# Performance work log

Hardware: AMD Instinct MI355X
Metric: run time of the kernel (lower is better)

## Reference

```python
import jax, jax.numpy as jnp
import numpy as np

D = 512
H = 8
W = 128  # window_size
HD = D // H
EPS = 1e-5


def _layernorm(x, g, b):
    mu = jnp.mean(x, axis=-1, keepdims=True)
    var = jnp.mean(jnp.square(x - mu), axis=-1, keepdims=True)
    return (x - mu) * jax.lax.rsqrt(var + EPS) * g + b


def setup_inputs() -> dict:
    key = jax.random.key(0)
    ks = jax.random.split(key, 6)
    B, S = 4, 8192
    src = jax.random.normal(ks[0], (B, S, D), jnp.float32)
    sc = 1.0 / np.sqrt(D)
    in_proj_w = jax.random.normal(ks[1], (3 * D, D), jnp.float32) * sc
    in_proj_b = jnp.zeros((3 * D,), jnp.float32)
    out_w = jax.random.normal(ks[2], (D, D), jnp.float32) * sc
    out_b = jnp.zeros((D,), jnp.float32)
    w1 = jax.random.normal(ks[3], (4 * D, D), jnp.float32) * sc
    b1 = jnp.zeros((4 * D,), jnp.float32)
    w2 = jax.random.normal(ks[4], (D, 4 * D), jnp.float32) * (1.0 / np.sqrt(4 * D))
    b2 = jnp.zeros((D,), jnp.float32)
    return {
        'src': src,
        'in_proj_w': in_proj_w, 'in_proj_b': in_proj_b,
        'out_w': out_w, 'out_b': out_b,
        'ln1_g': jnp.ones((D,), jnp.float32), 'ln1_b': jnp.zeros((D,), jnp.float32),
        'w1': w1, 'b1': b1, 'w2': w2, 'b2': b2,
        'ln2_g': jnp.ones((D,), jnp.float32), 'ln2_b': jnp.zeros((D,), jnp.float32),
    }


def reference(src, in_proj_w, in_proj_b, out_w, out_b, ln1_g, ln1_b,
              w1, b1, w2, b2, ln2_g, ln2_b):
    B, S, _ = src.shape
    nW = S // W
    x = src.reshape(B, nW, W, D)  # block-diagonal windows
    # packed qkv projection (torch MultiheadAttention in_proj)
    qkv = jnp.einsum('bnwd,ed->bnwe', x, in_proj_w) + in_proj_b
    q, k, v = jnp.split(qkv, 3, axis=-1)
    q = q.reshape(B, nW, W, H, HD)
    k = k.reshape(B, nW, W, H, HD)
    v = v.reshape(B, nW, W, H, HD)
    scores = jnp.einsum('bnqhd,bnkhd->bnhqk', q, k) / np.sqrt(HD)
    probs = jax.nn.softmax(scores, axis=-1)
    attn = jnp.einsum('bnhqk,bnkhd->bnqhd', probs, v).reshape(B, nW, W, D)
    attn = jnp.einsum('bnwd,ed->bnwe', attn, out_w) + out_b
    x = _layernorm(x + attn, ln1_g, ln1_b)
    ff = jnp.einsum('bnwf,df->bnwd', jax.nn.relu(jnp.einsum('bnwd,fd->bnwf', x, w1) + b1), w2) + b2
    x = _layernorm(x + ff, ln2_g, ln2_b)
    return x.reshape(B, S, D)
```

## Files before the change

### kernel.cpp

```cpp
#include <hip/hip_runtime.h>
#include <hip/hip_bf16.h>
#include <math.h>

typedef __bf16 bf16;
typedef bf16 bf16x8 __attribute__((ext_vector_type(8)));
typedef bf16 bf16x4 __attribute__((ext_vector_type(4)));
typedef float f32x4 __attribute__((ext_vector_type(4)));

#define MFMA16(a, b, c) __builtin_amdgcn_mfma_f32_16x16x32_bf16(a, b, c, 0, 0, 0)

__device__ __forceinline__ uint32_t swz(uint32_t base, uint32_t row, uint32_t rs, uint32_t cb) {
    return base + row * rs + (((cb >> 4) ^ (row & 7u)) << 4) + (cb & 15u);
}

__device__ __forceinline__ void gload16(const void* g, void* l) {
    __builtin_amdgcn_global_load_lds((const __attribute__((address_space(1))) void*)g,
                                     (__attribute__((address_space(3))) void*)l, 16, 0, 0);
}


__global__ void wcvt_kernel(const float* __restrict__ w0, const float* __restrict__ w1o,
                            const float* __restrict__ w1f, const float* __restrict__ w2f,
                            bf16* __restrict__ o) {
    int i = blockIdx.x * blockDim.x + threadIdx.x;
    const float* s;
    int soff, doff;
    if (i < 98304)        { int e = i * 8; s = w0; soff = e; doff = e; }
    else if (i < 131072)  { int e = (i - 98304) * 8; s = w1o; soff = e; doff = 786432 + e; }
    else if (i < 262144)  {
        int u = i - 131072;
        int tile = u >> 11, c = (u >> 9) & 3, nn = u & 511;
        int n = (tile >> 4) * 512 + nn;
        int k = (tile & 15) * 32 + c * 8;
        s = w1f; soff = n * 512 + k; doff = 1048576 + u * 8;
    } else {
        int u = i - 262144;
        int t = u >> 11, c = (u >> 9) & 3, nn = u & 511;
        int k = t * 32 + c * 8;
        s = w2f; soff = nn * 2048 + k; doff = 2097152 + u * 8;
    }
    float4 v0 = *(const float4*)(s + soff);
    float4 v1 = *(const float4*)(s + soff + 4);
    bf16x8 h = { (bf16)v0.x, (bf16)v0.y, (bf16)v0.z, (bf16)v0.w,
                 (bf16)v1.x, (bf16)v1.y, (bf16)v1.z, (bf16)v1.w };
    *(bf16x8*)(o + doff) = h;
}

__global__ void xcvt_kernel(float* __restrict__ src) {
    int row = blockIdx.x * 4 + (threadIdx.x >> 6);
    int l = threadIdx.x & 63;
    float* rp = src + (size_t)row * 512 + l * 8;
    float4 v0 = *(const float4*)rp;
    float4 v1 = *(const float4*)(rp + 4);
    asm volatile("s_waitcnt vmcnt(0)" ::: "memory");
    bf16x8 h = { (bf16)v0.x, (bf16)v0.y, (bf16)v0.z, (bf16)v0.w,
                 (bf16)v1.x, (bf16)v1.y, (bf16)v1.z, (bf16)v1.w };
    *(bf16x8*)((bf16*)(src + (size_t)row * 512) + l * 8) = h;
}

extern "C" __global__ __launch_bounds__(256, 3)
void qkv_kernel(const char* __restrict__ xb, const bf16* __restrict__ Wqkv,
                const float* __restrict__ bqkv, char* __restrict__ qOb,
                char* __restrict__ kvb) {
    extern __shared__ char smem[];
    const int tid = threadIdx.x;
    const int wid = tid >> 6, lane = tid & 63, l16 = lane & 15, quad = lane >> 4;
    const int wm = wid >> 1, wn = wid & 1;
    const int rb = blockIdx.x, cb = blockIdx.y;
    f32x4 acc[4][4];
#pragma unroll
    for (int i = 0; i < 4; ++i)
#pragma unroll
        for (int nt = 0; nt < 4; ++nt) acc[i][nt] = (f32x4){0.f, 0.f, 0.f, 0.f};

#pragma unroll 1
    for (int kstep = 0; kstep < 8; ++kstep) {
        {
            int lr = tid >> 1, half = tid & 1;
            const char* g = (const char*)(Wqkv + (size_t)(cb * 128 + lr) * 512 + kstep * 64 + half * 32);
#pragma unroll
            for (int c = 0; c < 4; ++c) {
                bf16x8 v = *(const bf16x8*)(g + c * 16);
                *(bf16x8*)(smem + swz(0, lr, 128, half * 64 + c * 16)) = v;
            }
        }
        __syncthreads();
#pragma unroll
        for (int k16 = 0; k16 < 2; ++k16) {
            bf16x8 a[4];
#pragma unroll
            for (int i = 0; i < 4; ++i) {
                int row = rb * 128 + wm * 64 + i * 16 + l16;
                a[i] = *(const bf16x8*)(xb + (size_t)row * 2048 + (kstep * 64 + k16 * 32 + quad * 8) * 2);
            }
#pragma unroll
            for (int nt = 0; nt < 4; ++nt) {
                bf16x8 b = *(bf16x8*)(smem + swz(0, wn * 64 + nt * 16 + l16, 128, k16 * 64 + quad * 16));
#pragma unroll
                for (int i = 0; i < 4; ++i) acc[i][nt] = MFMA16(a[i], b, acc[i][nt]);
            }
        }
        __syncthreads();
    }
    const uint32_t wb = (uint32_t)wid * 8192;
#pragma unroll
    for (int nt = 0; nt < 4; ++nt) {
        float bias = bqkv[cb * 128 + wn * 64 + nt * 16 + l16];
#pragma unroll
        for (int i = 0; i < 4; ++i)
#pragma unroll
            for (int r = 0; r < 4; ++r)
                *(bf16*)(smem + swz(wb, i * 16 + quad * 4 + r, 128, (nt * 16 + l16) * 2)) =
                    (bf16)(acc[i][nt][r] + bias);
    }
    asm volatile("s_waitcnt lgkmcnt(0)" ::: "memory");
    const int region = cb >> 2;
#pragma unroll
    for (int c = 0; c < 8; ++c) {
        int lr = c * 8 + (lane >> 3), ch = lane & 7;
        bf16x8 v = *(bf16x8*)(smem + swz(wb, lr, 128, ch * 16));
        int row_g = rb * 128 + wm * 64 + lr;
        int colb = (cb * 128 + wn * 64) * 2 + ch * 16;
        if (region == 0)      *(bf16x8*)(qOb + (size_t)row_g * 1024 + colb) = v;
        else if (region == 1) *(bf16x8*)(kvb + (size_t)row_g * 2048 + (colb - 1024)) = v;
        else                  *(bf16x8*)(kvb + (size_t)row_g * 2048 + 1024 + (colb - 2048)) = v;
    }
}

#define AVT 0u
#define ASCR 16384u
extern "C" __global__ __launch_bounds__(512, 4)
void attn_kernel(char* __restrict__ qOb, const char* __restrict__ kvb) {
    extern __shared__ char smem[];
    const int tid = threadIdx.x;
    const int wid = tid >> 6, lane = tid & 63, l16 = lane & 15, quad = lane >> 4;
    const int win = blockIdx.x >> 3, head = blockIdx.x & 7;
    const size_t wrow0 = (size_t)win * 128;
    f32x4 zero4 = { 0.f, 0.f, 0.f, 0.f };

    {
        int key = tid >> 2, d0 = (tid & 3) * 16;
        const char* vs = kvb + (wrow0 + key) * 2048 + 1024 + head * 128 + d0 * 2;
#pragma unroll
        for (int j = 0; j < 2; ++j) {
            bf16x8 v = *(const bf16x8*)(vs + j * 16);
#pragma unroll
            for (int e = 0; e < 8; ++e)
                *(bf16*)(smem + swz(AVT, d0 + j * 8 + e, 256, key * 2)) = v[e];
        }
    }
    __syncthreads();

    bf16x8 qf[2];
#pragma unroll
    for (int ks = 0; ks < 2; ++ks)
        qf[ks] = *(const bf16x8*)(qOb + (wrow0 + wid * 16 + l16) * 1024 + head * 128 + ks * 64 + quad * 16);

    f32x4 sa[8];
#pragma unroll
    for (int nt = 0; nt < 8; ++nt) sa[nt] = zero4;
#pragma unroll
    for (int nt = 0; nt < 8; ++nt)
#pragma unroll
        for (int ks = 0; ks < 2; ++ks) {
            bf16x8 kb = *(const bf16x8*)(kvb + (wrow0 + nt * 16 + l16) * 2048 + head * 128 + ks * 64 + quad * 16);
            sa[nt] = MFMA16(qf[ks], kb, sa[nt]);
        }
#pragma unroll
    for (int nt = 0; nt < 8; ++nt) sa[nt] *= 0.125f;
#pragma unroll
    for (int r = 0; r < 4; ++r) {
        float m = sa[0][r];
#pragma unroll
        for (int nt = 1; nt < 8; ++nt) m = fmaxf(m, sa[nt][r]);
#pragma unroll
        for (int sft = 1; sft < 16; sft <<= 1) m = fmaxf(m, __shfl_xor(m, sft, 64));
        float s = 0.f;
#pragma unroll
        for (int nt = 0; nt < 8; ++nt) {
            float e = __expf(sa[nt][r] - m);
            sa[nt][r] = e;
            s += e;
        }
#pragma unroll
        for (int sft = 1; sft < 16; sft <<= 1) s += __shfl_xor(s, sft, 64);
        float inv = 1.0f / s;
#pragma unroll
        for (int nt = 0; nt < 8; ++nt) sa[nt][r] *= inv;
    }

    const uint32_t sb = ASCR + (uint32_t)wid * 2048;
    bf16x8 pf[4];
#pragma unroll
    for (int hf = 0; hf < 2; ++hf) {
#pragma unroll
        for (int nt = 0; nt < 4; ++nt)
#pragma unroll
            for (int r = 0; r < 4; ++r)
                *(bf16*)(smem + swz(sb, quad * 4 + r, 128, (nt * 16 + l16) * 2)) = (bf16)sa[hf * 4 + nt][r];
        asm volatile("s_waitcnt lgkmcnt(0)" ::: "memory");
#pragma unroll
        for (int ks = 0; ks < 2; ++ks)
            pf[hf * 2 + ks] = *(bf16x8*)(smem + swz(sb, l16, 128, ks * 64 + quad * 16));
        asm volatile("s_waitcnt lgkmcnt(0)" ::: "memory");
    }

    f32x4 ov[4];
#pragma unroll
    for (int nt = 0; nt < 4; ++nt) {
        ov[nt] = zero4;
#pragma unroll
        for (int ks = 0; ks < 4; ++ks) {
            bf16x8 vb = *(bf16x8*)(smem + swz(AVT, nt * 16 + l16, 256, ks * 64 + quad * 16));
            ov[nt] = MFMA16(pf[ks], vb, ov[nt]);
        }
    }
#pragma unroll
    for (int hf = 0; hf < 2; ++hf) {
#pragma unroll
        for (int nt = 0; nt < 2; ++nt)
#pragma unroll
            for (int r = 0; r < 4; ++r)
                *(bf16*)(smem + swz(sb, quad * 4 + r, 128, (nt * 16 + l16) * 2)) = (bf16)ov[hf * 2 + nt][r];
        asm volatile("s_waitcnt lgkmcnt(0)" ::: "memory");
        {
            int row = lane >> 2, ch = lane & 3;
            bf16x8 v = *(bf16x8*)(smem + swz(sb, row, 128, ch * 16));
            *(bf16x8*)(qOb + (wrow0 + wid * 16 + row) * 1024 + head * 128 + hf * 64 + ch * 16) = v;
        }
        asm volatile("s_waitcnt lgkmcnt(0)" ::: "memory");
    }
}

extern "C" __global__ __launch_bounds__(256, 2)
void outproj_kernel(char* __restrict__ srcb, const char* __restrict__ qOb,
                    const bf16* __restrict__ Wout, const float* __restrict__ bout,
                    const float* __restrict__ g1, const float* __restrict__ be1) {
    extern __shared__ char smem[];
    const int tid = threadIdx.x;
    const int wid = tid >> 6, lane = tid & 63, l16 = lane & 15, quad = lane >> 4;
    const int mb = blockIdx.x;
    f32x4 acc[32];
#pragma unroll
    for (int nt = 0; nt < 32; ++nt) acc[nt] = (f32x4){0.f, 0.f, 0.f, 0.f};

#pragma unroll 1
    for (int kstep = 0; kstep < 8; ++kstep) {
        {
            int n0 = tid * 2;
#pragma unroll
            for (int rr = 0; rr < 2; ++rr) {
                int n = n0 + rr;
                const char* g = (const char*)(Wout + (size_t)n * 512 + kstep * 64);
#pragma unroll
                for (int c = 0; c < 8; ++c) {
                    bf16x8 v = *(const bf16x8*)(g + c * 16);
                    *(bf16x8*)(smem + swz(0, n, 128, c * 16)) = v;
                }
            }
        }
        __syncthreads();
#pragma unroll
        for (int k16 = 0; k16 < 2; ++k16) {
            bf16x8 a = *(const bf16x8*)(qOb + (size_t)(mb * 64 + wid * 16 + l16) * 1024 +
                                        (kstep * 64 + k16 * 32 + quad * 8) * 2);
#pragma unroll
            for (int nt = 0; nt < 32; ++nt) {
                bf16x8 b = *(bf16x8*)(smem + swz(0, nt * 16 + l16, 128, k16 * 64 + quad * 16));
                acc[nt] = MFMA16(a, b, acc[nt]);
            }
        }
        __syncthreads();
    }
#pragma unroll
    for (int nt = 0; nt < 32; ++nt) {
        int col = nt * 16 + l16;
        float bb = bout[col];
#pragma unroll
        for (int r = 0; r < 4; ++r) {
            int row = mb * 64 + wid * 16 + quad * 4 + r;
            float xv = (float)*(const bf16*)(srcb + (size_t)row * 2048 + col * 2);
            acc[nt][r] += bb + xv;
        }
    }
    const uint32_t wb = (uint32_t)wid * 16384;
#pragma unroll
    for (int r = 0; r < 4; ++r) {
        float s = 0.f, s2 = 0.f;
#pragma unroll
        for (int nt = 0; nt < 32; ++nt) {
            float v = acc[nt][r];
            s += v;
            s2 += v * v;
        }
#pragma unroll
        for (int sft = 1; sft < 16; sft <<= 1) {
            s += __shfl_xor(s, sft, 64);
            s2 += __shfl_xor(s2, sft, 64);
        }
        float mu = s * (1.0f / 512.0f);
        float var = s2 * (1.0f / 512.0f) - mu * mu;
        float rstd = rsqrtf(var + 1e-5f);
#pragma unroll
        for (int nt = 0; nt < 32; ++nt) {
            int col = nt * 16 + l16;
            float v = (acc[nt][r] - mu) * rstd * g1[col] + be1[col];
            *(bf16*)(smem + swz(wb, quad * 4 + r, 1024, col * 2)) = (bf16)v;
        }
    }
    asm volatile("s_waitcnt lgkmcnt(0)" ::: "memory");
#pragma unroll
    for (int t = 0; t < 16; ++t) {
        int row = (t >> 2) * 4 + (lane >> 4);
        int ch = (t & 3) * 16 + l16;
        bf16x8 v = *(bf16x8*)(smem + swz(wb, row, 1024, ch * 16));
        *(bf16x8*)(srcb + (size_t)(mb * 64 + wid * 16 + row) * 2048 + 1024 + ch * 16) = v;
    }
}

extern "C" __global__ __launch_bounds__(512, 2)
void ff1_kernel(char* __restrict__ srcb, const char* __restrict__ W1p,
                const float* __restrict__ b1, char* __restrict__ doutb,
                char* __restrict__ wsOb) {
    extern __shared__ char smem[];
    const int tid = threadIdx.x;
    const int w = tid >> 6, lane = tid & 63, l16 = lane & 15, quad = lane >> 4;
    const int wm = w >> 2, wn = w & 3;
    const int mb = blockIdx.x, cb = blockIdx.y;

    f32x4 acc[4][8];
#pragma unroll
    for (int i = 0; i < 4; ++i)
#pragma unroll
        for (int nt = 0; nt < 8; ++nt) acc[i][nt] = (f32x4){0.f, 0.f, 0.f, 0.f};

#define FF1_STAGE(buf, t)                                                              \
    {                                                                                  \
        int ca = w >> 1, rg = w & 1;             \
        gload16(srcb + (size_t)(mb * 128 + rg * 64 + lane) * 2048 + 1024 + (t) * 64 + ca * 16, \
                smem + (uint32_t)(buf) * 8192u + ca * 2048 + rg * 1024);               \
        _Pragma("unroll")                                                              \
        for (int j = 0; j < 4; ++j) {      \
            int idx = w * 4 + j, c = idx >> 3, ng = idx & 7;                           \
            gload16(W1p + (size_t)(cb * 16 + (t)) * 32768 + c * 8192 + ng * 1024 + lane * 16, \
                    smem + 16384u + (uint32_t)(buf) * 32768u + (uint32_t)c * 8192 + (uint32_t)ng * 1024); \
        }                                                                              \
    }

    FF1_STAGE(0, 0);
    __syncthreads();

#pragma unroll 1
    for (int t = 0; t < 16; ++t) {
        if (t < 15) FF1_STAGE((t + 1) & 1, t + 1);
        const uint32_t A0 = (uint32_t)(t & 1) * 8192u;
        const uint32_t B0 = 16384u + (uint32_t)(t & 1) * 32768u;
        bf16x8 a[4];
#pragma unroll
        for (int i = 0; i < 4; ++i)
            a[i] = *(const bf16x8*)(smem + A0 + quad * 2048 + (wm * 64 + i * 16 + l16) * 16);
#pragma unroll
        for (int nt = 0; nt < 8; ++nt) {
            bf16x8 b = *(const bf16x8*)(smem + B0 + quad * 8192 + (wn * 128 + nt * 16 + l16) * 16);
#pragma unroll
            for (int i = 0; i < 4; ++i) acc[i][nt] = MFMA16(a[i], b, acc[i][nt]);
        }
        __syncthreads();
    }
#undef FF1_STAGE

    const uint32_t sb = 16384u + (uint32_t)w * 4096u;
#pragma unroll
    for (int i = 0; i < 4; ++i) {
#pragma unroll
        for (int nt = 0; nt < 8; ++nt) {
            float bb = b1[cb * 512 + wn * 128 + nt * 16 + l16];
#pragma unroll
            for (int r = 0; r < 4; ++r)
                *(bf16*)(smem + swz(sb, quad * 4 + r, 256, (nt * 16 + l16) * 2)) =
                    (bf16)fmaxf(acc[i][nt][r] + bb, 0.0f);
        }
        asm volatile("s_waitcnt lgkmcnt(0)" ::: "memory");
#pragma unroll
        for (int j = 0; j < 4; ++j) {
            int uu = j * 64 + lane;
            int row = uu >> 4, ch = uu & 15;
            bf16x8 v = *(bf16x8*)(smem + swz(sb, row, 256, ch * 16));
            size_t row_g = (size_t)(mb * 128 + wm * 64 + i * 16 + row);
            int nb2 = wn * 256 + ch * 16;
            if (cb < 2)       *(bf16x8*)(doutb + row_g * 2048 + cb * 1024 + nb2) = v;
            else if (cb == 2) *(bf16x8*)(srcb + row_g * 2048 + nb2) = v;
            else              *(bf16x8*)(wsOb + row_g * 1024 + nb2) = v;
        }
        asm volatile("s_waitcnt lgkmcnt(0)" ::: "memory");
    }
}

extern "C" __global__ __launch_bounds__(512, 2)
void ff2_kernel(char* __restrict__ doutb, const char* __restrict__ srcb,
                const char* __restrict__ wsOb, const char* __restrict__ W2p,
                const float* __restrict__ b2, const float* __restrict__ g2,
                const float* __restrict__ be2) {
    extern __shared__ char smem[];
    const int tid = threadIdx.x;
    const int w = tid >> 6, lane = tid & 63, l16 = lane & 15, quad = lane >> 4;
    const int wm = w >> 2, wn = w & 3;
    const int mb = blockIdx.x;

    f32x4 acc[4][8];
#pragma unroll
    for (int i = 0; i < 4; ++i)
#pragma unroll
        for (int nt = 0; nt < 8; ++nt) acc[i][nt] = (f32x4){0.f, 0.f, 0.f, 0.f};

#define FF2_STAGE(buf, t)                                                              \
    {                                                                                  \
        const char* hb; int rstride, koffb;                                            \
        if ((t) < 32)      { hb = doutb; rstride = 2048; koffb = (t) * 64; }           \
        else if ((t) < 48) { hb = srcb;  rstride = 2048; koffb = ((t) - 32) * 64; }    \
        else               { hb = wsOb;  rstride = 1024; koffb = ((t) - 48) * 64; }    \
        int ca = w >> 1, rg = w & 1;           \
        gload16(hb + (size_t)(mb * 128 + rg * 64 + lane) * rstride + koffb + ca * 16,  \
                smem + (uint32_t)(buf) * 8192u + ca * 2048 + rg * 1024);               \
        _Pragma("unroll")                                                              \
        for (int j = 0; j < 4; ++j) {      \
            int idx = w * 4 + j, c = idx >> 3, ng = idx & 7;                           \
            gload16(W2p + (size_t)(t) * 32768 + c * 8192 + ng * 1024 + lane * 16,      \
                    smem + 16384u + (uint32_t)(buf) * 32768u + (uint32_t)c * 8192 + (uint32_t)ng * 1024); \
        }                                                                              \
    }

    FF2_STAGE(0, 0);
    __syncthreads();

#pragma unroll 1
    for (int t = 0; t < 64; ++t) {
        if (t < 63) FF2_STAGE((t + 1) & 1, t + 1);
        const uint32_t A0 = (uint32_t)(t & 1) * 8192u;
        const uint32_t B0 = 16384u + (uint32_t)(t & 1) * 32768u;
        bf16x8 a[4];
#pragma unroll
        for (int i = 0; i < 4; ++i)
            a[i] = *(const bf16x8*)(smem + A0 + quad * 2048 + (wm * 64 + i * 16 + l16) * 16);
#pragma unroll
        for (int nt = 0; nt < 8; ++nt) {
            bf16x8 b = *(const bf16x8*)(smem + B0 + quad * 8192 + (wn * 128 + nt * 16 + l16) * 16);
#pragma unroll
            for (int i = 0; i < 4; ++i) acc[i][nt] = MFMA16(a[i], b, acc[i][nt]);
        }
        __syncthreads();
    }
#undef FF2_STAGE

#pragma unroll
    for (int nt = 0; nt < 8; ++nt) {
        int col = wn * 128 + nt * 16 + l16;
        float bb = b2[col];
#pragma unroll
        for (int i = 0; i < 4; ++i)
#pragma unroll
            for (int r = 0; r < 4; ++r) {
                int row = mb * 128 + wm * 64 + i * 16 + quad * 4 + r;
                float x1v = (float)*(const bf16*)(srcb + (size_t)row * 2048 + 1024 + col * 2);
                acc[i][nt][r] += bb + x1v;
            }
    }
    float ps[4][4], ps2[4][4];
#pragma unroll
    for (int i = 0; i < 4; ++i)
#pragma unroll
        for (int r = 0; r < 4; ++r) {
            float s = 0.f, s2 = 0.f;
#pragma unroll
            for (int nt = 0; nt < 8; ++nt) {
                float v = acc[i][nt][r];
                s += v;
                s2 += v * v;
            }
#pragma unroll
            for (int sft = 1; sft < 16; sft <<= 1) {
                s += __shfl_xor(s, sft, 64);
                s2 += __shfl_xor(s2, sft, 64);
            }
            ps[i][r] = s;
            ps2[i][r] = s2;
        }
    if (l16 == 0) {
#pragma unroll
        for (int i = 0; i < 4; ++i)
#pragma unroll
            for (int r = 0; r < 4; ++r) {
                int row_l = wm * 64 + i * 16 + quad * 4 + r;
                *(float*)(smem + row_l * 32 + wn * 8) = ps[i][r];
                *(float*)(smem + row_l * 32 + wn * 8 + 4) = ps2[i][r];
            }
    }
    __syncthreads();
#pragma unroll
    for (int i = 0; i < 4; ++i)
#pragma unroll
        for (int r = 0; r < 4; ++r) {
            int row_l = wm * 64 + i * 16 + quad * 4 + r;
            float S = 0.f, S2 = 0.f;
#pragma unroll
            for (int w4 = 0; w4 < 4; ++w4) {
                S += *(const float*)(smem + row_l * 32 + w4 * 8);
                S2 += *(const float*)(smem + row_l * 32 + w4 * 8 + 4);
            }
            float mu = S * (1.0f / 512.0f);
            float var = S2 * (1.0f / 512.0f) - mu * mu;
            float rstd = rsqrtf(var + 1e-5f);
            size_t row = (size_t)(mb * 128 + row_l);
#pragma unroll
            for (int nt = 0; nt < 8; ++nt) {
                int col = wn * 128 + nt * 16 + l16;
                *(float*)(doutb + row * 2048 + col * 4) =
                    (acc[i][nt][r] - mu) * rstd * g2[col] + be2[col];
            }
        }
}

extern "C" void kernel_launch(void* const* d_in, const int* in_sizes, int n_in,
                              void* d_out, int out_size, void* d_ws, size_t ws_size,
                              hipStream_t stream) {
    (void)in_sizes; (void)n_in; (void)out_size; (void)ws_size;
    float* src = (float*)d_in[0];
    const float* ipw = (const float*)d_in[1];
    const float* ipb = (const float*)d_in[2];
    const float* ow  = (const float*)d_in[3];
    const float* ob  = (const float*)d_in[4];
    const float* g1  = (const float*)d_in[5];
    const float* be1 = (const float*)d_in[6];
    const float* w1  = (const float*)d_in[7];
    const float* b1  = (const float*)d_in[8];
    const float* w2  = (const float*)d_in[9];
    const float* b2  = (const float*)d_in[10];
    const float* g2  = (const float*)d_in[11];
    const float* be2 = (const float*)d_in[12];
    bf16* ws = (bf16*)d_ws;
    char* srcb = (char*)src;
    char* doutb = (char*)d_out;
    char* qOb = (char*)d_ws + 6291456;

    wcvt_kernel<<<1536, 256, 0, stream>>>(ipw, ow, w1, w2, ws);
    xcvt_kernel<<<8192, 256, 0, stream>>>(src);

    hipFuncSetAttribute((const void*)qkv_kernel, hipFuncAttributeMaxDynamicSharedMemorySize, 32768);
    hipFuncSetAttribute((const void*)attn_kernel, hipFuncAttributeMaxDynamicSharedMemorySize, 32768);
    hipFuncSetAttribute((const void*)outproj_kernel, hipFuncAttributeMaxDynamicSharedMemorySize, 65536);
    hipFuncSetAttribute((const void*)ff1_kernel, hipFuncAttributeMaxDynamicSharedMemorySize, 81920);
    hipFuncSetAttribute((const void*)ff2_kernel, hipFuncAttributeMaxDynamicSharedMemorySize, 81920);

    qkv_kernel<<<dim3(256, 12), 256, 32768, stream>>>(srcb, ws, ipb, qOb, doutb);
    attn_kernel<<<2048, 512, 32768, stream>>>(qOb, doutb);
    outproj_kernel<<<512, 256, 65536, stream>>>(srcb, qOb, ws + 786432, ob, g1, be1);
    ff1_kernel<<<dim3(256, 4), 512, 81920, stream>>>(srcb, (const char*)(ws + 1048576), b1, doutb, qOb);
    ff2_kernel<<<256, 512, 81920, stream>>>(doutb, srcb, qOb, (const char*)(ws + 2097152), b2, g2, be2);
}
```

Baseline: 595.9 us.

## Rewrite QKV and out-proj GEMMs with pre-tiled weights and double-buffered async LDS loads

The QKV and output-projection weights are now pre-packed into a K-tile-major bf16 layout during conversion. Both GEMMs switch to 512-thread blocks with 128x512 output tiles, staging A and B through double-buffered LDS using direct global-to-LDS loads. The next K tile is prefetched while MFMAs run on the current one. Out-proj also gains a cross-wave LDS reduction for the LayerNorm row statistics. In exchange, each block uses more LDS (80KB) and more accumulators, and the QKV grid drops from 3072 to 768 blocks, which may lower occupancy and leave some CUs underused.

```diff
diff --git a/kernel.cpp b/kernel.cpp
--- a/kernel.cpp
+++ b/kernel.cpp
@@ -19,15 +19,24 @@
 }
 
 
-__global__ void wcvt_kernel(const float* __restrict__ w0, const float* __restrict__ w1o,
+__global__ void wcvt_kernel(const float* __restrict__ wqkv, const float* __restrict__ wout,
                             const float* __restrict__ w1f, const float* __restrict__ w2f,
                             bf16* __restrict__ o) {
     int i = blockIdx.x * blockDim.x + threadIdx.x;
     const float* s;
     int soff, doff;
-    if (i < 98304)        { int e = i * 8; s = w0; soff = e; doff = e; }
-    else if (i < 131072)  { int e = (i - 98304) * 8; s = w1o; soff = e; doff = 786432 + e; }
-    else if (i < 262144)  {
+    if (i < 98304) {
+        int u = i;
+        int tile = u >> 11, c = (u >> 9) & 3, nn = u & 511;
+        int n = (tile >> 4) * 512 + nn;
+        int k = (tile & 15) * 32 + c * 8;
+        s = wqkv; soff = n * 512 + k; doff = u * 8;
+    } else if (i < 131072) {
+        int u = i - 98304;
+        int tile = u >> 11, c = (u >> 9) & 3, nn = u & 511;
+        int k = tile * 32 + c * 8;
+        s = wout; soff = nn * 512 + k; doff = 786432 + u * 8;
+    } else if (i < 262144) {
         int u = i - 131072;
         int tile = u >> 11, c = (u >> 9) & 3, nn = u & 511;
         int n = (tile >> 4) * 512 + nn;
@@ -58,72 +67,81 @@
     *(bf16x8*)((bf16*)(src + (size_t)row * 512) + l * 8) = h;
 }
 
-extern "C" __global__ __launch_bounds__(256, 3)
-void qkv_kernel(const char* __restrict__ xb, const bf16* __restrict__ Wqkv,
+extern "C" __global__ __launch_bounds__(512, 2)
+void qkv_kernel(const char* __restrict__ xb, const char* __restrict__ Wqkvp,
                 const float* __restrict__ bqkv, char* __restrict__ qOb,
                 char* __restrict__ kvb) {
     extern __shared__ char smem[];
     const int tid = threadIdx.x;
-    const int wid = tid >> 6, lane = tid & 63, l16 = lane & 15, quad = lane >> 4;
-    const int wm = wid >> 1, wn = wid & 1;
-    const int rb = blockIdx.x, cb = blockIdx.y;
-    f32x4 acc[4][4];
+    const int w = tid >> 6, lane = tid & 63, l16 = lane & 15, quad = lane >> 4;
+    const int wm = w >> 2, wn = w & 3;
+    const int mb = blockIdx.x, cb = blockIdx.y;
+
+    f32x4 acc[4][8];
 #pragma unroll
     for (int i = 0; i < 4; ++i)
 #pragma unroll
-        for (int nt = 0; nt < 4; ++nt) acc[i][nt] = (f32x4){0.f, 0.f, 0.f, 0.f};
+        for (int nt = 0; nt < 8; ++nt) acc[i][nt] = (f32x4){0.f, 0.f, 0.f, 0.f};
+
+#define QKV_STAGE(buf, t)                                                              \
+    {                                                                                  \
+        int ca = w >> 1, rg = w & 1;           \
+        gload16(xb + (size_t)(mb * 128 + rg * 64 + lane) * 2048 + (t) * 64 + ca * 16,  \
+                smem + (uint32_t)(buf) * 8192u + ca * 2048 + rg * 1024);               \
+        _Pragma("unroll")                                                              \
+        for (int j = 0; j < 4; ++j) {      \
+            int idx = w * 4 + j, c = idx >> 3, ng = idx & 7;                           \
+            gload16(Wqkvp + (size_t)(cb * 16 + (t)) * 32768 + c * 8192 + ng * 1024 + lane * 16, \
+                    smem + 16384u + (uint32_t)(buf) * 32768u + (uint32_t)c * 8192 + (uint32_t)ng * 1024); \
+        }                                                                              \
+    }
+
+    QKV_STAGE(0, 0);
+    __syncthreads();
 
 #pragma unroll 1
-    for (int kstep = 0; kstep < 8; ++kstep) {
-        {
-            int lr = tid >> 1, half = tid & 1;
-            const char* g = (const char*)(Wqkv + (size_t)(cb * 128 + lr) * 512 + kstep * 64 + half * 32);
-#pragma unroll
-            for (int c = 0; c < 4; ++c) {
-                bf16x8 v = *(const bf16x8*)(g + c * 16);
-                *(bf16x8*)(smem + swz(0, lr, 128, half * 64 + c * 16)) = v;
-            }
+    for (int t = 0; t < 16; ++t) {
+        if (t < 15) QKV_STAGE((t + 1) & 1, t + 1);
+        const uint32_t A0 = (uint32_t)(t & 1) * 8192u;
+        const uint32_t B0 = 16384u + (uint32_t)(t & 1) * 32768u;
+        bf16x8 a[4];
+#pragma unroll
+        for (int i = 0; i < 4; ++i)
+            a[i] = *(const bf16x8*)(smem + A0 + quad * 2048 + (wm * 64 + i * 16 + l16) * 16);
+#pragma unroll
+        for (int nt = 0; nt < 8; ++nt) {
+            bf16x8 b = *(const bf16x8*)(smem + B0 + quad * 8192 + (wn * 128 + nt * 16 + l16) * 16);
+#pragma unroll
+            for (int i = 0; i < 4; ++i) acc[i][nt] = MFMA16(a[i], b, acc[i][nt]);
         }
         __syncthreads();
-#pragma unroll
-        for (int k16 = 0; k16 < 2; ++k16) {
-            bf16x8 a[4];
-#pragma unroll
-            for (int i = 0; i < 4; ++i) {
-                int row = rb * 128 + wm * 64 + i * 16 + l16;
-                a[i] = *(const bf16x8*)(xb + (size_t)row * 2048 + (kstep * 64 + k16 * 32 + quad * 8) * 2);
-            }
-#pragma unroll
-            for (int nt = 0; nt < 4; ++nt) {
-                bf16x8 b = *(bf16x8*)(smem + swz(0, wn * 64 + nt * 16 + l16, 128, k16 * 64 + quad * 16));
-#pragma unroll
-                for (int i = 0; i < 4; ++i) acc[i][nt] = MFMA16(a[i], b, acc[i][nt]);
-            }
-        }
-        __syncthreads();
-    }
-    const uint32_t wb = (uint32_t)wid * 8192;
-#pragma unroll
-    for (int nt = 0; nt < 4; ++nt) {
-        float bias = bqkv[cb * 128 + wn * 64 + nt * 16 + l16];
-#pragma unroll
-        for (int i = 0; i < 4; ++i)
+    }
+#undef QKV_STAGE
+
+    const uint32_t sb = 16384u + (uint32_t)w * 4096u;
+#pragma unroll
+    for (int i = 0; i < 4; ++i) {
+#pragma unroll
+        for (int nt = 0; nt < 8; ++nt) {
+            float bb = bqkv[cb * 512 + wn * 128 + nt * 16 + l16];
 #pragma unroll
             for (int r = 0; r < 4; ++r)
-                *(bf16*)(smem + swz(wb, i * 16 + quad * 4 + r, 128, (nt * 16 + l16) * 2)) =
-                    (bf16)(acc[i][nt][r] + bias);
-    }
-    asm volatile("s_waitcnt lgkmcnt(0)" ::: "memory");
-    const int region = cb >> 2;
-#pragma unroll
-    for (int c = 0; c < 8; ++c) {
-        int lr = c * 8 + (lane >> 3), ch = lane & 7;
-        bf16x8 v = *(bf16x8*)(smem + swz(wb, lr, 128, ch * 16));
-        int row_g = rb * 128 + wm * 64 + lr;
-        int colb = (cb * 128 + wn * 64) * 2 + ch * 16;
-        if (region == 0)      *(bf16x8*)(qOb + (size_t)row_g * 1024 + colb) = v;
-        else if (region == 1) *(bf16x8*)(kvb + (size_t)row_g * 2048 + (colb - 1024)) = v;
-        else                  *(bf16x8*)(kvb + (size_t)row_g * 2048 + 1024 + (colb - 2048)) = v;
+                *(bf16*)(smem + swz(sb, quad * 4 + r, 256, (nt * 16 + l16) * 2)) =
+                    (bf16)(acc[i][nt][r] + bb);
+        }
+        asm volatile("s_waitcnt lgkmcnt(0)" ::: "memory");
+#pragma unroll
+        for (int j = 0; j < 4; ++j) {
+            int uu = j * 64 + lane;
+            int row = uu >> 4, ch = uu & 15;
+            bf16x8 v = *(bf16x8*)(smem + swz(sb, row, 256, ch * 16));
+            size_t row_g = (size_t)(mb * 128 + wm * 64 + i * 16 + row);
+            int nb2 = wn * 256 + ch * 16;
+            if (cb == 0)      *(bf16x8*)(qOb + row_g * 1024 + nb2) = v;
+            else if (cb == 1) *(bf16x8*)(kvb + row_g * 2048 + nb2) = v;
+            else              *(bf16x8*)(kvb + row_g * 2048 + 1024 + nb2) = v;
+        }
+        asm volatile("s_waitcnt lgkmcnt(0)" ::: "memory");
     }
 }
 
@@ -232,89 +250,133 @@
     }
 }
 
-extern "C" __global__ __launch_bounds__(256, 2)
+extern "C" __global__ __launch_bounds__(512, 2)
 void outproj_kernel(char* __restrict__ srcb, const char* __restrict__ qOb,
-                    const bf16* __restrict__ Wout, const float* __restrict__ bout,
+                    const char* __restrict__ Woutp, const float* __restrict__ bout,
                     const float* __restrict__ g1, const float* __restrict__ be1) {
     extern __shared__ char smem[];
     const int tid = threadIdx.x;
-    const int wid = tid >> 6, lane = tid & 63, l16 = lane & 15, quad = lane >> 4;
+    const int w = tid >> 6, lane = tid & 63, l16 = lane & 15, quad = lane >> 4;
+    const int wm = w >> 2, wn = w & 3;
     const int mb = blockIdx.x;
-    f32x4 acc[32];
-#pragma unroll
-    for (int nt = 0; nt < 32; ++nt) acc[nt] = (f32x4){0.f, 0.f, 0.f, 0.f};
+
+    f32x4 acc[4][8];
+#pragma unroll
+    for (int i = 0; i < 4; ++i)
+#pragma unroll
+        for (int nt = 0; nt < 8; ++nt) acc[i][nt] = (f32x4){0.f, 0.f, 0.f, 0.f};
+
+#define OP_STAGE(buf, t)                                                               \
+    {                                                                                  \
+        int ca = w >> 1, rg = w & 1;           \
+        gload16(qOb + (size_t)(mb * 128 + rg * 64 + lane) * 1024 + (t) * 64 + ca * 16, \
+                smem + (uint32_t)(buf) * 8192u + ca * 2048 + rg * 1024);               \
+        _Pragma("unroll")                                                              \
+        for (int j = 0; j < 4; ++j) {      \
+            int idx = w * 4 + j, c = idx >> 3, ng = idx & 7;                           \
+            gload16(Woutp + (size_t)(t) * 32768 + c * 8192 + ng * 1024 + lane * 16,    \
+                    smem + 16384u + (uint32_t)(buf) * 32768u + (uint32_t)c * 8192 + (uint32_t)ng * 1024); \
+        }                                                                              \
+    }
+
+    OP_STAGE(0, 0);
+    __syncthreads();
 
 #pragma unroll 1
-    for (int kstep = 0; kstep < 8; ++kstep) {
-        {
-            int n0 = tid * 2;
-#pragma unroll
-            for (int rr = 0; rr < 2; ++rr) {
-                int n = n0 + rr;
-                const char* g = (const char*)(Wout + (size_t)n * 512 + kstep * 64);
-#pragma unroll
-                for (int c = 0; c < 8; ++c) {
-                    bf16x8 v = *(const bf16x8*)(g + c * 16);
-                    *(bf16x8*)(smem + swz(0, n, 128, c * 16)) = v;
-                }
-            }
+    for (int t = 0; t < 16; ++t) {
+        if (t < 15) OP_STAGE((t + 1) & 1, t + 1);
+        const uint32_t A0 = (uint32_t)(t & 1) * 8192u;
+        const uint32_t B0 = 16384u + (uint32_t)(t & 1) * 32768u;
+        bf16x8 a[4];
+#pragma unroll
+        for (int i = 0; i < 4; ++i)
+            a[i] = *(const bf16x8*)(smem + A0 + quad * 2048 + (wm * 64 + i * 16 + l16) * 16);
+#pragma unroll
+        for (int nt = 0; nt < 8; ++nt) {
+            bf16x8 b = *(const bf16x8*)(smem + B0 + quad * 8192 + (wn * 128 + nt * 16 + l16) * 16);
+#pragma unroll
+            for (int i = 0; i < 4; ++i) acc[i][nt] = MFMA16(a[i], b, acc[i][nt]);
         }
         __syncthreads();
-#pragma unroll
-        for (int k16 = 0; k16 < 2; ++k16) {
-            bf16x8 a = *(const bf16x8*)(qOb + (size_t)(mb * 64 + wid * 16 + l16) * 1024 +
-                                        (kstep * 64 + k16 * 32 + quad * 8) * 2);
-#pragma unroll
-            for (int nt = 0; nt < 32; ++nt) {
-                bf16x8 b = *(bf16x8*)(smem + swz(0, nt * 16 + l16, 128, k16 * 64 + quad * 16));
-                acc[nt] = MFMA16(a, b, acc[nt]);
-            }
-        }
-        __syncthreads();
-    }
-#pragma unroll
-    for (int nt = 0; nt < 32; ++nt) {
-        int col = nt * 16 + l16;
+    }
+#undef OP_STAGE
+
+#pragma unroll
+    for (int nt = 0; nt < 8; ++nt) {
+        int col = wn * 128 + nt * 16 + l16;
         float bb = bout[col];
 #pragma unroll
+        for (int i = 0; i < 4; ++i)
+#pragma unroll
+            for (int r = 0; r < 4; ++r) {
+                int row = mb * 128 + wm * 64 + i * 16 + quad * 4 + r;
+                float xv = (float)*(const bf16*)(srcb + (size_t)row * 2048 + col * 2);
+                acc[i][nt][r] += bb + xv;
+            }
+    }
+    float ps[4][4], ps2[4][4];
+#pragma unroll
+    for (int i = 0; i < 4; ++i)
+#pragma unroll
         for (int r = 0; r < 4; ++r) {
-            int row = mb * 64 + wid * 16 + quad * 4 + r;
-            float xv = (float)*(const bf16*)(srcb + (size_t)row * 2048 + col * 2);
-            acc[nt][r] += bb + xv;
-        }
-    }
-    const uint32_t wb = (uint32_t)wid * 16384;
-#pragma unroll
-    for (int r = 0; r < 4; ++r) {
-        float s = 0.f, s2 = 0.f;
-#pragma unroll
-        for (int nt = 0; nt < 32; ++nt) {
-            float v = acc[nt][r];
-            s += v;
-            s2 += v * v;
-        }
-#pragma unroll
-        for (int sft = 1; sft < 16; sft <<= 1) {
-            s += __shfl_xor(s, sft, 64);
-            s2 += __shfl_xor(s2, sft, 64);
-        }
-        float mu = s * (1.0f / 512.0f);
-        float var = s2 * (1.0f / 512.0f) - mu * mu;
-        float rstd = rsqrtf(var + 1e-5f);
-#pragma unroll
-        for (int nt = 0; nt < 32; ++nt) {
-            int col = nt * 16 + l16;
-            float v = (acc[nt][r] - mu) * rstd * g1[col] + be1[col];
-            *(bf16*)(smem + swz(wb, quad * 4 + r, 1024, col * 2)) = (bf16)v;
-        }
-    }
-    asm volatile("s_waitcnt lgkmcnt(0)" ::: "memory");
-#pragma unroll
-    for (int t = 0; t < 16; ++t) {
-        int row = (t >> 2) * 4 + (lane >> 4);
-        int ch = (t & 3) * 16 + l16;
-        bf16x8 v = *(bf16x8*)(smem + swz(wb, row, 1024, ch * 16));
-        *(bf16x8*)(srcb + (size_t)(mb * 64 + wid * 16 + row) * 2048 + 1024 + ch * 16) = v;
+            float s = 0.f, s2 = 0.f;
+#pragma unroll
+            for (int nt = 0; nt < 8; ++nt) {
+                float v = acc[i][nt][r];
+                s += v;
+                s2 += v * v;
+            }
+#pragma unroll
+            for (int sft = 1; sft < 16; sft <<= 1) {
+                s += __shfl_xor(s, sft, 64);
+                s2 += __shfl_xor(s2, sft, 64);
+            }
+            ps[i][r] = s;
+            ps2[i][r] = s2;
+        }
+    if (l16 == 0) {
+#pragma unroll
+        for (int i = 0; i < 4; ++i)
+#pragma unroll
+            for (int r = 0; r < 4; ++r) {
+                int row_l = wm * 64 + i * 16 + quad * 4 + r;
+                *(float*)(smem + row_l * 32 + wn * 8) = ps[i][r];
+                *(float*)(smem + row_l * 32 + wn * 8 + 4) = ps2[i][r];
+            }
+    }
+    __syncthreads();
+    const uint32_t sb = 16384u + (uint32_t)w * 4096u;
+#pragma unroll
+    for (int i = 0; i < 4; ++i) {
+#pragma unroll
+        for (int r = 0; r < 4; ++r) {
+            int row_l = wm * 64 + i * 16 + quad * 4 + r;
+            float S = 0.f, S2 = 0.f;
+#pragma unroll
+            for (int w4 = 0; w4 < 4; ++w4) {
+                S += *(const float*)(smem + row_l * 32 + w4 * 8);
+                S2 += *(const float*)(smem + row_l * 32 + w4 * 8 + 4);
+            }
+            float mu = S * (1.0f / 512.0f);
+            float var = S2 * (1.0f / 512.0f) - mu * mu;
+            float rstd = rsqrtf(var + 1e-5f);
+#pragma unroll
+            for (int nt = 0; nt < 8; ++nt) {
+                int col = wn * 128 + nt * 16 + l16;
+                float v = (acc[i][nt][r] - mu) * rstd * g1[col] + be1[col];
+                *(bf16*)(smem + swz(sb, quad * 4 + r, 256, (nt * 16 + l16) * 2)) = (bf16)v;
+            }
+        }
+        asm volatile("s_waitcnt lgkmcnt(0)" ::: "memory");
+#pragma unroll
+        for (int j = 0; j < 4; ++j) {
+            int uu = j * 64 + lane;
+            int row = uu >> 4, ch = uu & 15;
+            bf16x8 v = *(bf16x8*)(smem + swz(sb, row, 256, ch * 16));
+            *(bf16x8*)(srcb + (size_t)(mb * 128 + wm * 64 + i * 16 + row) * 2048 + 1024 +
+                       wn * 256 + ch * 16) = v;
+        }
+        asm volatile("s_waitcnt lgkmcnt(0)" ::: "memory");
     }
 }
 
@@ -545,15 +607,15 @@
     wcvt_kernel<<<1536, 256, 0, stream>>>(ipw, ow, w1, w2, ws);
     xcvt_kernel<<<8192, 256, 0, stream>>>(src);
 
-    hipFuncSetAttribute((const void*)qkv_kernel, hipFuncAttributeMaxDynamicSharedMemorySize, 32768);
+    hipFuncSetAttribute((const void*)qkv_kernel, hipFuncAttributeMaxDynamicSharedMemorySize, 81920);
     hipFuncSetAttribute((const void*)attn_kernel, hipFuncAttributeMaxDynamicSharedMemorySize, 32768);
-    hipFuncSetAttribute((const void*)outproj_kernel, hipFuncAttributeMaxDynamicSharedMemorySize, 65536);
+    hipFuncSetAttribute((const void*)outproj_kernel, hipFuncAttributeMaxDynamicSharedMemorySize, 81920);
     hipFuncSetAttribute((const void*)ff1_kernel, hipFuncAttributeMaxDynamicSharedMemorySize, 81920);
     hipFuncSetAttribute((const void*)ff2_kernel, hipFuncAttributeMaxDynamicSharedMemorySize, 81920);
 
-    qkv_kernel<<<dim3(256, 12), 256, 32768, stream>>>(srcb, ws, ipb, qOb, doutb);
+    qkv_kernel<<<dim3(256, 3), 512, 81920, stream>>>(srcb, (const char*)ws, ipb, qOb, doutb);
     attn_kernel<<<2048, 512, 32768, stream>>>(qOb, doutb);
-    outproj_kernel<<<512, 256, 65536, stream>>>(srcb, qOb, ws + 786432, ob, g1, be1);
+    outproj_kernel<<<256, 512, 81920, stream>>>(srcb, qOb, (const char*)(ws + 786432), ob, g1, be1);
     ff1_kernel<<<dim3(256, 4), 512, 81920, stream>>>(srcb, (const char*)(ws + 1048576), b1, doutb, qOb);
     ff2_kernel<<<256, 512, 81920, stream>>>(doutb, srcb, qOb, (const char*)(ws + 2097152), b2, g2, be2);
 }
```

Measured after the change: 524.4 us. 1.14x faster.
